# Performance work log

Hardware: AMD Instinct MI355X
Metric: run time of the kernel (lower is better)

Reference implementation:

```python
import jax, jax.numpy as jnp
import numpy as np

B, D_IN, LAT, C = 16384, 512, 64, 8
HID = [1024, 512, 256]

def _lin(k, fi, fo, scale=0.02):
    k1, k2 = jax.random.split(k)
    return jax.random.normal(k1, (fi, fo), jnp.float32) * scale, jax.random.normal(k2, (fo,), jnp.float32) * scale

def _lin_c(k, fi, fo, scale=0.02):
    k1, k2 = jax.random.split(k)
    return jax.random.normal(k1, (C, fi, fo), jnp.float32) * scale, jax.random.normal(k2, (C, fo), jnp.float32) * scale

def setup_inputs() -> dict:
    key = jax.random.key(0)
    ks = jax.random.split(key, 16)
    x = jax.random.normal(ks[0], (B, D_IN), jnp.float32)
    cluster_labels = jax.random.randint(ks[1], (B,), 0, C, jnp.int32)
    eps = jax.random.normal(ks[2], (B, LAT), jnp.float32)
    # encoder: shared(512->1024), unshared(1024->512), shared(512->256)
    enc_W0, enc_b0 = _lin(ks[3], D_IN, HID[0])
    enc_Wu, enc_bu = _lin_c(ks[4], HID[0], HID[1])
    enc_W2, enc_b2 = _lin(ks[5], HID[1], HID[2])
    # shared latent heads
    mu_W, mu_b = _lin(ks[6], HID[2], LAT)
    lv_W, lv_b = _lin(ks[7], HID[2], LAT)
    # decoder (hidden_dims reversed = [256,512,1024]): unshared(64->256), shared(256->512), unshared(512->1024)
    dec_Wu0, dec_bu0 = _lin_c(ks[8], LAT, HID[2])
    dec_W1, dec_b1 = _lin(ks[9], HID[2], HID[1])
    dec_Wu2, dec_bu2 = _lin_c(ks[10], HID[1], HID[0])
    # per-cluster final layer (1024 -> input_dim), no activation (all-continuous)
    fin_W, fin_b = _lin_c(ks[11], HID[0], D_IN)
    return dict(x=x, cluster_labels=cluster_labels, eps=eps,
                enc_W0=enc_W0, enc_b0=enc_b0, enc_Wu=enc_Wu, enc_bu=enc_bu,
                enc_W2=enc_W2, enc_b2=enc_b2, mu_W=mu_W, mu_b=mu_b,
                lv_W=lv_W, lv_b=lv_b, dec_Wu0=dec_Wu0, dec_bu0=dec_bu0,
                dec_W1=dec_W1, dec_b1=dec_b1, dec_Wu2=dec_Wu2, dec_bu2=dec_bu2,
                fin_W=fin_W, fin_b=fin_b)

def _unshared(h, W, b, labels):
    # per-cluster GEMM then row-wise combine (mask-based dispatch, no row reorder)
    y = jnp.einsum('bi,cio->bco', h, W) + b[None]  # [B, C, out]
    return jnp.take_along_axis(y, labels[:, None, None], axis=1)[:, 0, :]

def reference(x, cluster_labels, eps,
              enc_W0, enc_b0, enc_Wu, enc_bu, enc_W2, enc_b2,
              mu_W, mu_b, lv_W, lv_b,
              dec_Wu0, dec_bu0, dec_W1, dec_b1, dec_Wu2, dec_bu2,
              fin_W, fin_b):
    lbl = cluster_labels.astype(jnp.int32)
    # encoder
    h = jax.nn.relu(x @ enc_W0 + enc_b0)
    h = jax.nn.relu(_unshared(h, enc_Wu, enc_bu, lbl))
    h = jax.nn.relu(h @ enc_W2 + enc_b2)
    mu = h @ mu_W + mu_b
    logvar = h @ lv_W + lv_b
    # reparameterize
    z = mu + jnp.exp(0.5 * logvar) * eps
    # decoder
    h = jax.nn.relu(_unshared(z, dec_Wu0, dec_bu0, lbl))
    h = jax.nn.relu(h @ dec_W1 + dec_b1)
    h = jax.nn.relu(_unshared(h, dec_Wu2, dec_bu2, lbl))
    # per-cluster final output layer (identity activation: all-continuous)
    recon = _unshared(h, fin_W, fin_b, lbl)
    return recon
```

## Files before the change

### kernel.cpp

```cpp
#include <hip/hip_runtime.h>

typedef _Float16 f16;
typedef __attribute__((ext_vector_type(8))) _Float16 f16x8;
typedef __attribute__((ext_vector_type(4))) _Float16 f16x4;
typedef __attribute__((ext_vector_type(4))) float    f32x4;

#define B_ROWS 16384
#define MPAD   17408
#define MTILES 136
#define NBLK   64

typedef __attribute__((address_space(1))) void as1_void;
typedef __attribute__((address_space(3))) void as3_void;

__device__ __forceinline__ void gl_lds16(const void* g, void* l) {
    __builtin_amdgcn_global_load_lds((const as1_void*)g, (as3_void*)l, 16, 0, 0);
}


__global__ __launch_bounds__(256) void k_prep(const int* __restrict__ lbl, int* __restrict__ blockhist,
                                              int* __restrict__ rowmap,
                                              const float* __restrict__ mb_, const float* __restrict__ lb_,
                                              float* __restrict__ bz, f16* __restrict__ zerob) {
    int b = blockIdx.x, t = threadIdx.x;
    int i = b * 256 + t;
    rowmap[i] = -1;
    if (b < NBLK) {
        __shared__ int h[8];
        if (t < 8) h[t] = 0;
        __syncthreads();
        atomicAdd(&h[lbl[i]], 1);
        __syncthreads();
        if (t < 8) blockhist[b * 8 + t] = h[t];
    } else if (b == NBLK) {
        if (t < 64) zerob[t] = (f16)0.f;
        if (t < 64) bz[t] = mb_[t];
        else if (t < 128) bz[t] = lb_[t - 64];
    }
}

__global__ void k_offsets(const int* __restrict__ blockhist, int* offs, int* tilec, int* blockbase) {
    __shared__ int tot[8];
    __shared__ int so[9];
    int t = threadIdx.x;
    if (t < 8) {
        int s = 0;
        for (int b = 0; b < NBLK; ++b) s += blockhist[b * 8 + t];
        tot[t] = s;
    }
    __syncthreads();
    if (t == 0) {
        int o = 0;
        for (int c = 0; c < 8; ++c) { so[c] = o; o += (tot[c] + 127) & ~127; }
        so[8] = o;
        for (int c = 0; c < 9; ++c) offs[c] = so[c];
    }
    __syncthreads();
    if (t < 8) {
        int run = so[t];
        for (int b = 0; b < NBLK; ++b) {
            blockbase[b * 8 + t] = run;
            run += blockhist[b * 8 + t];
        }
    }
    if (t < MTILES) {
        int row = t * 128, c = 7;
        for (int cc = 0; cc < 8; ++cc)
            if (row >= so[cc] && row < so[cc + 1]) c = cc;
        tilec[t] = c;
    }
}

__global__ __launch_bounds__(256) void k_scatter(const int* __restrict__ lbl,
                                                 const int* __restrict__ blockbase,
                                                 int* __restrict__ rowmap) {
    __shared__ int cur[8];
    if (threadIdx.x < 8) cur[threadIdx.x] = blockbase[blockIdx.x * 8 + threadIdx.x];
    __syncthreads();
    int i = blockIdx.x * 256 + threadIdx.x;
    int c = lbl[i];
    int pos = atomicAdd(&cur[c], 1);
    rowmap[pos] = i;
}


struct Seg { const float* s; f16* d; int K, N, b0, nx, ny; long sCS, dCS; };
struct SegTab { Seg g[10]; };

__global__ __launch_bounds__(256) void k_trans(SegTab tab, const float* __restrict__ x, f16* __restrict__ xh) {
    int bid = blockIdx.x;
    int t = threadIdx.x;
    if (bid < tab.g[1].b0) {
        size_t i = (size_t)bid * 256 + t;
        float4 a = ((const float4*)x)[2 * i];
        float4 b = ((const float4*)x)[2 * i + 1];
        f16x8 o = {(f16)a.x, (f16)a.y, (f16)a.z, (f16)a.w,
                   (f16)b.x, (f16)b.y, (f16)b.z, (f16)b.w};
        ((f16x8*)xh)[i] = o;
        return;
    }
    int s = 9;
    while (bid < tab.g[s].b0) --s;
    Seg sg = tab.g[s];
    int lb = bid - sg.b0;
    int nxy = sg.nx * sg.ny;
    int z = lb / nxy; int r = lb - z * nxy;
    int by = r / sg.nx; int bx = r - by * sg.nx;
    const float* src = sg.s + (size_t)z * sg.sCS;
    f16* dst = sg.d + (size_t)z * sg.dCS;
    int n0 = bx * 64, k0 = by * 64;
    __shared__ float ld[64][64];
    int cr = t >> 4, cc = (t & 15) * 4;
    #pragma unroll
    for (int i = 0; i < 4; ++i) {
        int rr = cr + 16 * i;
        float4 v = *(const float4*)(src + (size_t)(k0 + rr) * sg.N + n0 + cc);
        *(float4*)&ld[rr][(((cc >> 2) ^ (rr & 15)) << 2)] = v;
    }
    __syncthreads();
    #pragma unroll
    for (int p = 0; p < 2; ++p) {
        int G = p * 256 + t;
        int n = G >> 3, gg = G & 7;
        f16x8 o;
        #pragma unroll
        for (int j = 0; j < 8; ++j) {
            int kk = gg * 8 + j;
            o[j] = (f16)ld[kk][(((n >> 2) ^ (kk & 15)) << 2) | (n & 3)];
        }
        *(f16x8*)(dst + (size_t)(n0 + n) * sg.K + k0 + gg * 8) = o;
    }
}


template<int GATHER, int PERW, int RELU, int EPI>
__global__ __launch_bounds__(256) void gemm_k(
    const f16* __restrict__ A, const f16* __restrict__ Wt,
    const float* __restrict__ bias, f16* __restrict__ Out, float* __restrict__ OutF,
    const float* __restrict__ eps,
    const int* __restrict__ rowmap, const int* __restrict__ tilec,
    const f16* __restrict__ zerobuf, int K, int N)
{
    __shared__ __align__(16) char smem[65536];
    const int tid  = threadIdx.x;
    const int wave = tid >> 6;
    const int lane = tid & 63;

    const int id  = blockIdx.x;
    const int xcd = id & 7;
    const int jj  = id >> 3;
    const int tm  = (jj % 17) * 8 + xcd;
    const int tn  = jj / 17;
    const int r0 = tm * 128, n0 = tn * 128;

    const f16* wb = Wt;
    const float* bb = bias;
    if (PERW) {
        int c = tilec[tm];
        wb += (size_t)c * K * N;
        bb += (size_t)c * N;
    }

    const int srow = tid >> 3;
    const int sg   = tid & 7;
    const int xk16 = (sg ^ (srow & 7)) * 16;
    const size_t rowB = (size_t)K * 2;
    const size_t passB = 32 * rowB;

    const char* pa[4]; size_t stepA[4];
    #pragma unroll
    for (int p = 0; p < 4; ++p) {
        int gr = r0 + p * 32 + srow;
        if (GATHER) {
            int g = rowmap[gr];
            if (g >= 0) { pa[p] = (const char*)(A + (size_t)g * K) + xk16; stepA[p] = 128; }
            else        { pa[p] = (const char*)zerobuf;                    stepA[p] = 0;   }
        } else {
            pa[p] = (const char*)(A + (size_t)gr * K) + xk16; stepA[p] = 128;
        }
    }
    const char* pb = (const char*)(wb + (size_t)(n0 + srow) * K) + xk16;

    const int mb = (wave >> 1) * 64;
    const int nb = (wave & 1) * 64;
    const int quad = lane >> 4;
    const int r16  = lane & 15;
    const int key  = r16 & 7;

    float bv[4];
    #pragma unroll
    for (int j = 0; j < 4; ++j) bv[j] = bb[n0 + nb + j * 16 + r16];

    f32x4 acc[4][4];
    #pragma unroll
    for (int i = 0; i < 4; ++i)
        #pragma unroll
        for (int j = 0; j < 4; ++j)
            acc[i][j] = (f32x4){0.f, 0.f, 0.f, 0.f};

    auto stage = [&](char* dst) {
        #pragma unroll
        for (int p = 0; p < 4; ++p)
            gl_lds16(pa[p], dst + p * 4096 + wave * 1024);
        #pragma unroll
        for (int p = 0; p < 4; ++p)
            gl_lds16(pb + p * passB, dst + 16384 + p * 4096 + wave * 1024);
        #pragma unroll
        for (int p = 0; p < 4; ++p) pa[p] += stepA[p];
        pb += 128;
    };

    auto compute = [&](const char* base) {
        const char* lA = base;
        const char* lB = base + 16384;
        #pragma unroll
        for (int kk = 0; kk < 2; ++kk) {
            const int off = ((kk * 4 + quad) ^ key) * 16;
            f16x8 af[4], bf[4];
            #pragma unroll
            for (int i = 0; i < 4; ++i)
                af[i] = *(const f16x8*)(lA + (mb + i * 16 + r16) * 128 + off);
            #pragma unroll
            for (int j = 0; j < 4; ++j)
                bf[j] = *(const f16x8*)(lB + (nb + j * 16 + r16) * 128 + off);
            #pragma unroll
            for (int i = 0; i < 4; ++i)
                #pragma unroll
                for (int j = 0; j < 4; ++j)
                    acc[i][j] = __builtin_amdgcn_mfma_f32_16x16x32_f16(af[i], bf[j], acc[i][j], 0, 0, 0);
        }
    };

    const int nk = K >> 6;
    stage(smem);
    int cur = 0;
    for (int kb = 0; kb < nk - 1; ++kb) {
        stage(smem + ((cur ^ 1) << 15));
        asm volatile("s_waitcnt vmcnt(8)" ::: "memory");
        __builtin_amdgcn_s_barrier();
        compute(smem + (cur << 15));
        __builtin_amdgcn_s_barrier();
        cur ^= 1;
    }
    asm volatile("s_waitcnt vmcnt(0)" ::: "memory");
    __builtin_amdgcn_s_barrier();
    compute(smem + (cur << 15));

    if (EPI == 2) {
        __syncthreads();
        #pragma unroll
        for (int i = 0; i < 4; ++i) {
            #pragma unroll
            for (int r = 0; r < 4; ++r) {
                int lr = mb + i * 16 + quad * 4 + r;
                #pragma unroll
                for (int j = 0; j < 4; ++j) {
                    int lc = nb + j * 16 + r16;
                    float v = acc[i][j][r] + bv[j];
                    *(f16*)(smem + lr * 256 + ((((lc >> 3) ^ (lr & 7))) << 4) + ((lc & 7) << 1)) = (f16)v;
                }
            }
        }
        __syncthreads();
        const int col = tid & 63;
        const int rb  = tid >> 6;
        for (int rr = 0; rr < 32; ++rr) {
            int row = rb * 32 + rr;
            int g = rowmap[r0 + row];
            float e = (g >= 0) ? eps[(size_t)g * 64 + col] : 0.f;
            float mu = (float)*(const f16*)(smem + row * 256 + ((((col >> 3) ^ (row & 7))) << 4) + ((col & 7) << 1));
            int c2 = col + 64;
            float lv = (float)*(const f16*)(smem + row * 256 + ((((c2 >> 3) ^ (row & 7))) << 4) + ((c2 & 7) << 1));
            Out[(size_t)(r0 + row) * 64 + col] = (f16)(mu + expf(0.5f * lv) * e);
        }
        return;
    }

    #pragma unroll
    for (int i = 0; i < 4; ++i) {
        #pragma unroll
        for (int r = 0; r < 4; ++r) {
            int orow = r0 + mb + i * 16 + quad * 4 + r;
            int g = 0;
            if (EPI == 1) g = rowmap[orow];
            #pragma unroll
            for (int j = 0; j < 4; ++j) {
                int ocol = n0 + nb + j * 16 + r16;
                float v = acc[i][j][r] + bv[j];
                if (RELU) v = fmaxf(v, 0.f);
                if (EPI == 1) {
                    if (g >= 0) OutF[(size_t)g * N + ocol] = v;
                } else {
                    Out[(size_t)orow * N + ocol] = (f16)v;
                }
            }
        }
    }
}


extern "C" void kernel_launch(void* const* d_in, const int* in_sizes, int n_in,
                              void* d_out, int out_size, void* d_ws, size_t ws_size,
                              hipStream_t stream) {
    const float* x      = (const float*)d_in[0];
    const int*   lbl    = (const int*)  d_in[1];
    const float* eps    = (const float*)d_in[2];
    const float* enc_W0 = (const float*)d_in[3];
    const float* enc_b0 = (const float*)d_in[4];
    const float* enc_Wu = (const float*)d_in[5];
    const float* enc_bu = (const float*)d_in[6];
    const float* enc_W2 = (const float*)d_in[7];
    const float* enc_b2 = (const float*)d_in[8];
    const float* mu_W   = (const float*)d_in[9];
    const float* mu_b   = (const float*)d_in[10];
    const float* lv_W   = (const float*)d_in[11];
    const float* lv_b   = (const float*)d_in[12];
    const float* dWu0   = (const float*)d_in[13];
    const float* dbu0   = (const float*)d_in[14];
    const float* dW1    = (const float*)d_in[15];
    const float* db1    = (const float*)d_in[16];
    const float* dWu2   = (const float*)d_in[17];
    const float* dbu2   = (const float*)d_in[18];
    const float* finW   = (const float*)d_in[19];
    const float* finb   = (const float*)d_in[20];
    float* out = (float*)d_out;
    (void)in_sizes; (void)n_in; (void)out_size; (void)ws_size;

    char* base = (char*)d_ws;
    size_t off = 0;
    auto alloc = [&](size_t bytes) { char* r = base + off; off = (off + bytes + 255) & ~(size_t)255; return r; };
    f16* xh     = (f16*)alloc((size_t)B_ROWS * 512 * 2);
    f16* buf1   = (f16*)alloc((size_t)MPAD * 1024 * 2);
    f16* buf2   = (f16*)alloc((size_t)MPAD * 512 * 2);
    f16* buf3   = (f16*)alloc((size_t)MPAD * 256 * 2);
    f16* zb     = (f16*)alloc((size_t)MPAD * 64 * 2);
    f16* w0t    = (f16*)alloc(1024ul * 512 * 2);
    f16* wut    = (f16*)alloc(8ul * 512 * 1024 * 2);
    f16* w2t    = (f16*)alloc(256ul * 512 * 2);
    f16* wzt    = (f16*)alloc(128ul * 256 * 2);
    f16* wd0t   = (f16*)alloc(8ul * 256 * 64 * 2);
    f16* wd1t   = (f16*)alloc(512ul * 256 * 2);
    f16* wd2t   = (f16*)alloc(8ul * 1024 * 512 * 2);
    f16* wft    = (f16*)alloc(8ul * 512 * 1024 * 2);
    float* bz   = (float*)alloc(128 * 4);
    int* rowmap = (int*)alloc(MPAD * 4);
    int* blockhist = (int*)alloc(NBLK * 8 * 4);
    int* blockbase = (int*)alloc(NBLK * 8 * 4);
    int* offs   = (int*)alloc(64);
    int* tilec  = (int*)alloc(MTILES * 4);
    f16* zerob  = (f16*)alloc(256);

    k_prep<<<MPAD / 256, 256, 0, stream>>>(lbl, blockhist, rowmap, mu_b, lv_b, bz, zerob);
    k_offsets<<<1, 256, 0, stream>>>(blockhist, offs, tilec, blockbase);
    k_scatter<<<NBLK, 256, 0, stream>>>(lbl, blockbase, rowmap);

    SegTab tab;
    int b0 = B_ROWS * 512 / 8 / 256;
    auto seg = [&](int i, const float* s, f16* d, int K, int N, int nz, long sCS, long dCS) {
        int nx = N / 64, ny = K / 64;
        tab.g[i] = Seg{s, d, K, N, b0, nx, ny, sCS, dCS};
        b0 += nx * ny * nz;
    };
    tab.g[0] = Seg{nullptr, nullptr, 0, 0, 0, 0, 0, 0, 0};
    seg(1, enc_W0, w0t, 512, 1024, 1, 0, 0);
    seg(2, enc_Wu, wut, 1024, 512, 8, 1024l * 512, 512l * 1024);
    seg(3, enc_W2, w2t, 512, 256, 1, 0, 0);
    seg(4, mu_W, wzt, 256, 64, 1, 0, 0);
    seg(5, lv_W, wzt + 64 * 256, 256, 64, 1, 0, 0);
    seg(6, dWu0, wd0t, 64, 256, 8, 64l * 256, 256l * 64);
    seg(7, dW1, wd1t, 256, 512, 1, 0, 0);
    seg(8, dWu2, wd2t, 512, 1024, 8, 512l * 1024, 1024l * 512);
    seg(9, finW, wft, 1024, 512, 8, 1024l * 512, 512l * 1024);
    k_trans<<<b0, 256, 0, stream>>>(tab, x, xh);

    gemm_k<1,0,1,0><<<MTILES * 8, 256, 0, stream>>>(xh,   w0t,  enc_b0, buf1, nullptr, nullptr, rowmap, tilec, zerob, 512, 1024);
    gemm_k<0,1,1,0><<<MTILES * 4, 256, 0, stream>>>(buf1, wut,  enc_bu, buf2, nullptr, nullptr, rowmap, tilec, zerob, 1024, 512);
    gemm_k<0,0,1,0><<<MTILES * 2, 256, 0, stream>>>(buf2, w2t,  enc_b2, buf3, nullptr, nullptr, rowmap, tilec, zerob, 512, 256);
    gemm_k<0,0,0,2><<<MTILES * 1, 256, 0, stream>>>(buf3, wzt,  bz,     zb,   nullptr, eps,     rowmap, tilec, zerob, 256, 128);
    gemm_k<0,1,1,0><<<MTILES * 2, 256, 0, stream>>>(zb,   wd0t, dbu0,   buf3, nullptr, nullptr, rowmap, tilec, zerob, 64, 256);
    gemm_k<0,0,1,0><<<MTILES * 4, 256, 0, stream>>>(buf3, wd1t, db1,    buf2, nullptr, nullptr, rowmap, tilec, zerob, 256, 512);
    gemm_k<0,1,1,0><<<MTILES * 8, 256, 0, stream>>>(buf2, wd2t, dbu2,   buf1, nullptr, nullptr, rowmap, tilec, zerob, 512, 1024);
    gemm_k<0,1,0,1><<<MTILES * 4, 256, 0, stream>>>(buf1, wft,  finb,   nullptr, out,  nullptr, rowmap, tilec, zerob, 1024, 512);
}
```

Baseline: 361.4 us.

## Add 128x256-tile 512-thread GEMM for N=1024 layers and grid-stride transpose kernel

Introduces a new GEMM kernel with 512 threads and 128x256 output tiles, double-buffered global-to-LDS loads and MFMA 16x16x32, used for the two layers with N=1024. This halves the grid for those layers and raises weight reuse per loaded A tile. The prep/transpose kernel is also changed to a persistent grid-stride loop over 512 blocks instead of one block per tile. The risks are lower occupancy from the larger per-thread accumulator set and a non-coalesced scalar f16 epilogue store.

```diff
diff --git a/kernel.cpp b/kernel.cpp
--- a/kernel.cpp
+++ b/kernel.cpp
@@ -87,48 +87,165 @@
 struct Seg { const float* s; f16* d; int K, N, b0, nx, ny; long sCS, dCS; };
 struct SegTab { Seg g[10]; };
 
-__global__ __launch_bounds__(256) void k_trans(SegTab tab, const float* __restrict__ x, f16* __restrict__ xh) {
-    int bid = blockIdx.x;
+__global__ __launch_bounds__(256) void k_trans(SegTab tab, const float* __restrict__ x,
+                                               f16* __restrict__ xh, int nvb) {
     int t = threadIdx.x;
-    if (bid < tab.g[1].b0) {
-        size_t i = (size_t)bid * 256 + t;
-        float4 a = ((const float4*)x)[2 * i];
-        float4 b = ((const float4*)x)[2 * i + 1];
-        f16x8 o = {(f16)a.x, (f16)a.y, (f16)a.z, (f16)a.w,
-                   (f16)b.x, (f16)b.y, (f16)b.z, (f16)b.w};
-        ((f16x8*)xh)[i] = o;
-        return;
-    }
-    int s = 9;
-    while (bid < tab.g[s].b0) --s;
-    Seg sg = tab.g[s];
-    int lb = bid - sg.b0;
-    int nxy = sg.nx * sg.ny;
-    int z = lb / nxy; int r = lb - z * nxy;
-    int by = r / sg.nx; int bx = r - by * sg.nx;
-    const float* src = sg.s + (size_t)z * sg.sCS;
-    f16* dst = sg.d + (size_t)z * sg.dCS;
-    int n0 = bx * 64, k0 = by * 64;
     __shared__ float ld[64][64];
-    int cr = t >> 4, cc = (t & 15) * 4;
+    for (int vb = blockIdx.x; vb < nvb; vb += gridDim.x) {
+        if (vb < tab.g[1].b0) {
+            size_t i = (size_t)vb * 256 + t;
+            float4 a = ((const float4*)x)[2 * i];
+            float4 b = ((const float4*)x)[2 * i + 1];
+            f16x8 o = {(f16)a.x, (f16)a.y, (f16)a.z, (f16)a.w,
+                       (f16)b.x, (f16)b.y, (f16)b.z, (f16)b.w};
+            ((f16x8*)xh)[i] = o;
+            continue;
+        }
+        int s = 9;
+        while (vb < tab.g[s].b0) --s;
+        Seg sg = tab.g[s];
+        int lb = vb - sg.b0;
+        int nxy = sg.nx * sg.ny;
+        int z = lb / nxy; int r = lb - z * nxy;
+        int by = r / sg.nx; int bx = r - by * sg.nx;
+        const float* src = sg.s + (size_t)z * sg.sCS;
+        f16* dst = sg.d + (size_t)z * sg.dCS;
+        int n0 = bx * 64, k0 = by * 64;
+        int cr = t >> 4, cc = (t & 15) * 4;
+        #pragma unroll
+        for (int i = 0; i < 4; ++i) {
+            int rr = cr + 16 * i;
+            float4 v = *(const float4*)(src + (size_t)(k0 + rr) * sg.N + n0 + cc);
+            *(float4*)&ld[rr][(((cc >> 2) ^ (rr & 15)) << 2)] = v;
+        }
+        __syncthreads();
+        #pragma unroll
+        for (int p = 0; p < 2; ++p) {
+            int G = p * 256 + t;
+            int n = G >> 3, gg = G & 7;
+            f16x8 o;
+            #pragma unroll
+            for (int j = 0; j < 8; ++j) {
+                int kk = gg * 8 + j;
+                o[j] = (f16)ld[kk][(((n >> 2) ^ (kk & 15)) << 2) | (n & 3)];
+            }
+            *(f16x8*)(dst + (size_t)(n0 + n) * sg.K + k0 + gg * 8) = o;
+        }
+        __syncthreads();
+    }
+}
+
+
+template<int GATHER, int PERW>
+__global__ __launch_bounds__(512, 4) void gemm2_k(
+    const f16* __restrict__ A, const f16* __restrict__ Wt,
+    const float* __restrict__ bias, f16* __restrict__ Out,
+    const int* __restrict__ rowmap, const int* __restrict__ tilec,
+    const f16* __restrict__ zerobuf, int K, int N)
+{
+    __shared__ __align__(16) char smem[49152];
+    const int tid  = threadIdx.x;
+    const int wave = tid >> 6;
+    const int lane = tid & 63;
+
+    const int id  = blockIdx.x;
+    const int xcd = id & 7;
+    const int jj  = id >> 3;
+    const int tm  = (jj % 17) * 8 + xcd;
+    const int tn  = jj / 17;
+    const int r0 = tm * 128, n0 = tn * 256;
+
+    const f16* wb = Wt;
+    const float* bb = bias;
+    if (PERW) {
+        int c = tilec[tm];
+        wb += (size_t)c * K * N;
+        bb += (size_t)c * N;
+    }
+
+    const int srow = tid >> 2, sg = tid & 3;
+    const int xk16 = (sg ^ ((srow >> 1) & 3)) * 16;
+    const size_t rowB = (size_t)K * 2;
+
+    const char* pa; size_t stepA;
+    if (GATHER) {
+        int g = rowmap[r0 + srow];
+        if (g >= 0) { pa = (const char*)A + (size_t)g * rowB + xk16; stepA = 64; }
+        else        { pa = (const char*)zerobuf;                     stepA = 0;  }
+    } else {
+        pa = (const char*)A + (size_t)(r0 + srow) * rowB + xk16; stepA = 64;
+    }
+    const char* pb = (const char*)wb + (size_t)(n0 + srow) * rowB + xk16;
+    const size_t pbOff = 128 * rowB;
+
+    const int mb = (wave >> 2) * 64;
+    const int nb = (wave & 3) * 64;
+    const int quad = lane >> 4;
+    const int r16  = lane & 15;
+    const int off  = (quad ^ ((r16 >> 1) & 3)) * 16;
+
+    float bv[4];
+    #pragma unroll
+    for (int j = 0; j < 4; ++j) bv[j] = bb[n0 + nb + j * 16 + r16];
+
+    f32x4 acc[4][4];
+    #pragma unroll
+    for (int i = 0; i < 4; ++i)
+        #pragma unroll
+        for (int j = 0; j < 4; ++j)
+            acc[i][j] = (f32x4){0.f, 0.f, 0.f, 0.f};
+
+    auto stage = [&](char* dst) {
+        gl_lds16(pa,           dst +         wave * 1024);
+        gl_lds16(pb,           dst + 8192  + wave * 1024);
+        gl_lds16(pb + pbOff,   dst + 16384 + wave * 1024);
+        pa += stepA; pb += 64;
+    };
+
+    auto compute = [&](const char* base) {
+        const char* lA = base;
+        const char* lB = base + 8192;
+        f16x8 af[4], bf[4];
+        #pragma unroll
+        for (int i = 0; i < 4; ++i)
+            af[i] = *(const f16x8*)(lA + (mb + i * 16 + r16) * 64 + off);
+        #pragma unroll
+        for (int j = 0; j < 4; ++j)
+            bf[j] = *(const f16x8*)(lB + (nb + j * 16 + r16) * 64 + off);
+        #pragma unroll
+        for (int i = 0; i < 4; ++i)
+            #pragma unroll
+            for (int j = 0; j < 4; ++j)
+                acc[i][j] = __builtin_amdgcn_mfma_f32_16x16x32_f16(af[i], bf[j], acc[i][j], 0, 0, 0);
+    };
+
+    const int nk = K >> 5;
+    stage(smem);
+    int cur = 0;
+    for (int kb = 0; kb < nk - 1; ++kb) {
+        stage(smem + (cur ^ 1) * 24576);
+        asm volatile("s_waitcnt vmcnt(3)" ::: "memory");
+        __builtin_amdgcn_s_barrier();
+        compute(smem + cur * 24576);
+        __builtin_amdgcn_s_barrier();
+        cur ^= 1;
+    }
+    asm volatile("s_waitcnt vmcnt(0)" ::: "memory");
+    __builtin_amdgcn_s_barrier();
+    compute(smem + cur * 24576);
+
     #pragma unroll
     for (int i = 0; i < 4; ++i) {
-        int rr = cr + 16 * i;
-        float4 v = *(const float4*)(src + (size_t)(k0 + rr) * sg.N + n0 + cc);
-        *(float4*)&ld[rr][(((cc >> 2) ^ (rr & 15)) << 2)] = v;
-    }
-    __syncthreads();
-    #pragma unroll
-    for (int p = 0; p < 2; ++p) {
-        int G = p * 256 + t;
-        int n = G >> 3, gg = G & 7;
-        f16x8 o;
-        #pragma unroll
-        for (int j = 0; j < 8; ++j) {
-            int kk = gg * 8 + j;
-            o[j] = (f16)ld[kk][(((n >> 2) ^ (kk & 15)) << 2) | (n & 3)];
-        }
-        *(f16x8*)(dst + (size_t)(n0 + n) * sg.K + k0 + gg * 8) = o;
+        #pragma unroll
+        for (int r = 0; r < 4; ++r) {
+            int orow = r0 + mb + i * 16 + quad * 4 + r;
+            #pragma unroll
+            for (int j = 0; j < 4; ++j) {
+                int ocol = n0 + nb + j * 16 + r16;
+                float v = fmaxf(acc[i][j][r] + bv[j], 0.f);
+                Out[(size_t)orow * N + ocol] = (f16)v;
+            }
+        }
     }
 }
 
@@ -371,14 +488,14 @@
     seg(7, dW1, wd1t, 256, 512, 1, 0, 0);
     seg(8, dWu2, wd2t, 512, 1024, 8, 512l * 1024, 1024l * 512);
     seg(9, finW, wft, 1024, 512, 8, 1024l * 512, 512l * 1024);
-    k_trans<<<b0, 256, 0, stream>>>(tab, x, xh);
-
-    gemm_k<1,0,1,0><<<MTILES * 8, 256, 0, stream>>>(xh,   w0t,  enc_b0, buf1, nullptr, nullptr, rowmap, tilec, zerob, 512, 1024);
+    k_trans<<<512, 256, 0, stream>>>(tab, x, xh, b0);
+
+    gemm2_k<1,0><<<MTILES * 4, 512, 0, stream>>>(xh,   w0t,  enc_b0, buf1, rowmap, tilec, zerob, 512, 1024);
     gemm_k<0,1,1,0><<<MTILES * 4, 256, 0, stream>>>(buf1, wut,  enc_bu, buf2, nullptr, nullptr, rowmap, tilec, zerob, 1024, 512);
     gemm_k<0,0,1,0><<<MTILES * 2, 256, 0, stream>>>(buf2, w2t,  enc_b2, buf3, nullptr, nullptr, rowmap, tilec, zerob, 512, 256);
     gemm_k<0,0,0,2><<<MTILES * 1, 256, 0, stream>>>(buf3, wzt,  bz,     zb,   nullptr, eps,     rowmap, tilec, zerob, 256, 128);
     gemm_k<0,1,1,0><<<MTILES * 2, 256, 0, stream>>>(zb,   wd0t, dbu0,   buf3, nullptr, nullptr, rowmap, tilec, zerob, 64, 256);
     gemm_k<0,0,1,0><<<MTILES * 4, 256, 0, stream>>>(buf3, wd1t, db1,    buf2, nullptr, nullptr, rowmap, tilec, zerob, 256, 512);
-    gemm_k<0,1,1,0><<<MTILES * 8, 256, 0, stream>>>(buf2, wd2t, dbu2,   buf1, nullptr, nullptr, rowmap, tilec, zerob, 512, 1024);
+    gemm2_k<0,1><<<MTILES * 4, 512, 0, stream>>>(buf2, wd2t, dbu2,   buf1, rowmap, tilec, zerob, 512, 1024);
     gemm_k<0,1,0,1><<<MTILES * 4, 256, 0, stream>>>(buf1, wft,  finb,   nullptr, out,  nullptr, rowmap, tilec, zerob, 1024, 512);
 }
```

Result: no change. 362.8 us (+0.4%).
